# Kernel optimization log

Measured on AMD Instinct MI355X. Metric: run time of the kernel, lower is better.

The kernel has to match this reference:

```python
import jax, jax.numpy as jnp
import numpy as np

N1, N2 = 8192, 8192
E1, E2 = 131072, 131072
F_IN, NH, B = 64, 128, 256
D6 = 6 * NH  # set2set in_channels = 768


def _gcn(x, W, b, src, dst, ew, n):
    xw = x @ W
    loop = jnp.arange(n)
    s = jnp.concatenate([src, loop])
    d = jnp.concatenate([dst, loop])
    w = jnp.concatenate([ew, jnp.ones((n,), ew.dtype)])
    deg = jax.ops.segment_sum(w, d, num_segments=n)
    dinv = jnp.where(deg > 0, jax.lax.rsqrt(deg), 0.0)
    norm = (dinv[s] * w * dinv[d])[:, None]
    return jax.ops.segment_sum(xw[s] * norm, d, num_segments=n) + b


def _leaky(x):
    return jax.nn.leaky_relu(x, 0.2)


def _l2norm(x):
    return x / jnp.maximum(jnp.linalg.norm(x, axis=1, keepdims=True), 1e-12)


def _set2set(x, batch, nseg, Wih, Whh, bih, bhh, steps=2):
    # Set2Set pooling: LSTM(input=2d, hidden=d) + segment softmax attention
    d = x.shape[1]
    h = jnp.zeros((nseg, d), x.dtype)
    c = jnp.zeros((nseg, d), x.dtype)
    q_star = jnp.zeros((nseg, 2 * d), x.dtype)
    for _ in range(steps):
        gates = q_star @ Wih.T + h @ Whh.T + bih + bhh
        gi, gf, gg, go = jnp.split(gates, 4, axis=1)  # torch LSTM gate order i,f,g,o
        c = jax.nn.sigmoid(gf) * c + jax.nn.sigmoid(gi) * jnp.tanh(gg)
        h = jax.nn.sigmoid(go) * jnp.tanh(c)
        e = jnp.sum(x * h[batch], axis=1)
        emax = jax.ops.segment_max(e, batch, num_segments=nseg)
        ee = jnp.exp(e - emax[batch])
        a = ee / jax.ops.segment_sum(ee, batch, num_segments=nseg)[batch]
        r = jax.ops.segment_sum(a[:, None] * x, batch, num_segments=nseg)
        q_star = jnp.concatenate([h, r], axis=1)
    return q_star


def setup_inputs():
    key = jax.random.key(0)
    ks = jax.random.split(key, 20)
    f32 = jnp.float32

    def xav(k, shp):
        fan_in, fan_out = shp[-1], shp[0] if len(shp) == 2 else shp[-1]
        lim = float(np.sqrt(6.0 / (shp[0] + shp[1])))
        return jax.random.uniform(k, shp, f32, -lim, lim)

    inp = {}
    inp["features_1"] = jax.random.normal(ks[0], (N1, F_IN), f32)
    inp["features_2"] = jax.random.normal(ks[1], (N2, F_IN), f32)
    inp["edge_attr_1"] = jax.random.uniform(ks[2], (E1,), f32)
    inp["edge_attr_2"] = jax.random.uniform(ks[3], (E2,), f32)
    inp["W0"] = xav(ks[4], (F_IN, NH)); inp["b0"] = jnp.zeros((NH,), f32)
    inp["W1"] = xav(ks[5], (NH, NH)); inp["b1"] = jnp.zeros((NH,), f32)
    inp["W2"] = xav(ks[6], (NH, NH)); inp["b2"] = jnp.zeros((NH,), f32)
    inp["Wih"] = xav(ks[7], (4 * D6, 2 * D6)); inp["bih"] = jnp.zeros((4 * D6,), f32)
    inp["Whh"] = xav(ks[8], (4 * D6, D6)); inp["bhh"] = jnp.zeros((4 * D6,), f32)
    inp["Wp1"] = xav(ks[9], (256, 4 * D6)); inp["bp1"] = jnp.zeros((256,), f32)
    inp["Wp2"] = xav(ks[10], (128, 256)); inp["bp2"] = jnp.zeros((128,), f32)
    inp["Wp3"] = xav(ks[11], (1, 128)); inp["bp3"] = jnp.zeros((1,), f32)
    inp["edge_index_1"] = jax.random.randint(ks[12], (2, E1), 0, N1)
    inp["edge_index_2"] = jax.random.randint(ks[13], (2, E2), 0, N2)
    inp["batch_1"] = jnp.sort(jax.random.randint(ks[14], (N1,), 0, B))
    inp["batch_2"] = jnp.sort(jax.random.randint(ks[15], (N2,), 0, B))
    return inp


def reference(features_1, features_2, edge_attr_1, edge_attr_2,
              W0, b0, W1, b1, W2, b2, Wih, bih, Whh, bhh,
              Wp1, bp1, Wp2, bp2, Wp3, bp3,
              edge_index_1, edge_index_2, batch_1, batch_2):
    s1, d1 = edge_index_1[0], edge_index_1[1]
    s2, d2 = edge_index_2[0], edge_index_2[1]

    f1a = _leaky(_gcn(features_1, W0, b0, s1, d1, edge_attr_1, N1))
    f2a = _leaky(_gcn(features_2, W0, b0, s2, d2, edge_attr_2, N2))
    f1b = _leaky(_gcn(f1a, W1, b1, s1, d1, edge_attr_1, N1))
    f2b = _leaky(_gcn(f2a, W1, b1, s2, d2, edge_attr_2, N2))
    f1c = _leaky(_gcn(f1b, W2, b2, s1, d1, edge_attr_1, N1))
    f2c = _leaky(_gcn(f2b, W2, b2, s2, d2, edge_attr_2, N2))
    h1 = jnp.concatenate([f1a, f1b, f1c], axis=1)  # [N1, 3*NH]
    h2 = jnp.concatenate([f2a, f2b, f2c], axis=1)  # [N2, 3*NH]

    # interaction: cosine-sim map masked to same-graph pairs (len_map)
    ns = _l2norm(h1)
    nv = _l2norm(h2)
    mask = (batch_1[:, None] == batch_2[None, :]).astype(ns.dtype)  # [N1, N2]
    imap = (ns @ nv.T) * mask
    f1 = jnp.concatenate([ns, imap @ nv], axis=1)      # [N1, 6*NH]
    f2 = jnp.concatenate([nv, imap.T @ ns], axis=1)    # [N2, 6*NH]

    g1 = _set2set(f1, batch_1, B, Wih, Whh, bih, bhh)  # [B, 12*NH]
    g2 = _set2set(f2, batch_2, B, Wih, Whh, bih, bhh)  # [B, 12*NH]
    z = jnp.concatenate([g1, g2], axis=1)              # [B, 24*NH]
    z = jax.nn.relu(z @ Wp1.T + bp1)
    z = jax.nn.relu(z @ Wp2.T + bp2)
    z = z @ Wp3.T + bp3
    return jax.nn.sigmoid(z).reshape(-1)
```

## Files before the change

kernel.cpp:

```cpp
#include <hip/hip_runtime.h>
#include <cmath>

#define N_NODES 8192
#define N_EDGES 131072
#define NB      256
#define NH      128
#define D3      384
#define D6      768
#define SMM     96
#define SLD     104
#define MAXDEG  64

typedef __attribute__((ext_vector_type(8))) short short8v;
typedef __attribute__((ext_vector_type(4))) float f32x4;
typedef unsigned short bf16t;

__device__ __forceinline__ float sigf(float x){ return 1.0f/(1.0f+__expf(-x)); }
__device__ __forceinline__ unsigned short f2bf(float x){
  unsigned u = __float_as_uint(x);
  unsigned r = u + 0x7FFF + ((u>>16)&1);
  return (unsigned short)(r>>16);
}
__device__ __forceinline__ float bfl(unsigned u){ return __uint_as_float(u<<16); }
__device__ __forceinline__ float bfh(unsigned u){ return __uint_as_float(u & 0xFFFF0000u); }
__device__ __forceinline__ float b2f(bf16t u){ return __uint_as_float(((unsigned)u)<<16); }
__device__ __forceinline__ float h0val(const float* bih, const float* bhh, int j){
  float c = sigf(bih[j]+bhh[j]) * tanhf(bih[2*D6+j]+bhh[2*D6+j]);
  return sigf(bih[3*D6+j]+bhh[3*D6+j]) * tanhf(c);
}

__device__ __forceinline__ void xw_body(int vb, int t,
    const bf16t* __restrict__ x1, const bf16t* __restrict__ x2, int xs, int K,
    const bf16t* __restrict__ Wt, bf16t* __restrict__ xw1, bf16t* __restrict__ xw2){
  int side = vb >> 8; int b = vb & 255;
  const bf16t* x = side? x2:x1;
  bf16t* xw = side? xw2:xw1;
  int w = t>>6, lane = t&63;
  int lm = lane&15, quad = lane>>4;
  int r0 = b*32 + (w>>1)*16;
  int c0 = (w&1)*64;
  const bf16t* a = x + (size_t)(r0+lm)*xs + quad*8;
  f32x4 acc[4] = {};
  for (int k=0;k<K;k+=32){
    short8v af = *(const short8v*)(a + k);
    #pragma unroll
    for (int ni=0;ni<4;ni++){
      short8v bf = *(const short8v*)(Wt + (size_t)(c0+ni*16+lm)*K + quad*8 + k);
      acc[ni] = __builtin_amdgcn_mfma_f32_16x16x32_bf16(af, bf, acc[ni], 0,0,0);
    }
  }
  #pragma unroll
  for (int ni=0;ni<4;ni++)
    #pragma unroll
    for (int r=0;r<4;r++){
      int row = r0 + quad*4 + r, col = c0 + ni*16 + lm;
      xw[(size_t)row*NH + col] = f2bf(acc[ni][r]);
    }
}


__global__ __launch_bounds__(256) void k_setup(
    const float* __restrict__ Wih, short* __restrict__ Wih16,
    const float* __restrict__ Wp1, short* __restrict__ Wp116,
    const float* __restrict__ fe1, const float* __restrict__ fe2,
    short* __restrict__ xf1, short* __restrict__ xf2,
    const float* __restrict__ W0, const float* __restrict__ W1, const float* __restrict__ W2,
    bf16t* __restrict__ Wt,
    const float* __restrict__ Whh, const float* __restrict__ bih, const float* __restrict__ bhh,
    float* __restrict__ cvec,
    float* deg1, float* deg2, int* ecur1, int* ecur2, int* cnt1, int* cnt2){
  __shared__ float hs[D6];
  int b = blockIdx.x, tid = threadIdx.x;
  if (b < 2304){
    int t = b*256 + tid;
    int n = t/192, q = t - n*192;
    float4 v = ((const float4*)(Wih + (size_t)n*1536 + 768))[q];
    short4 o = { (short)f2bf(v.x), (short)f2bf(v.y), (short)f2bf(v.z), (short)f2bf(v.w) };
    ((short4*)Wih16)[t] = o;
  } else if (b < 3072){
    int t = (b-2304)*256 + tid;
    float4 v = ((const float4*)Wp1)[t];
    short4 o = { (short)f2bf(v.x), (short)f2bf(v.y), (short)f2bf(v.z), (short)f2bf(v.w) };
    ((short4*)Wp116)[t] = o;
  } else if (b < 4096){
    int t = (b-3072)*256 + tid;
    int side = t >= 131072; int i = t & 131071;
    float4 v = ((const float4*)(side? fe2:fe1))[i];
    short4 o = { (short)f2bf(v.x), (short)f2bf(v.y), (short)f2bf(v.z), (short)f2bf(v.w) };
    ((short4*)(side? xf2:xf1))[i] = o;
  } else if (b < 4099){
    int l = b - 4096;
    const float* W = (l==0)? W0 : ((l==1)? W1 : W2);
    int K = (l==0)? 64 : 128;
    bf16t* dst = Wt + ((l==0)? 0 : ((l==1)? 128*64 : 128*64+128*128));
    for (int idx = tid; idx < 128*K; idx += 256){
      int n = idx / K, k = idx - n*K;
      dst[idx] = f2bf(W[k*NH + n]);
    }
  } else if (b < 4867){
    int j0 = (b - 4099)*4;
    for (int k=tid; k<D6; k+=256) hs[k] = h0val(bih,bhh,k);
    __syncthreads();
    int w = tid>>6, lane = tid&63;
    int j = j0 + w;
    const float4* wi = (const float4*)(Wih + (size_t)j*(2*D6));
    const float4* wh = (const float4*)(Whh + (size_t)j*D6);
    const float4* h4 = (const float4*)hs;
    float acc=0;
    #pragma unroll
    for (int m=0;m<3;m++){
      float4 hv = h4[m*64+lane];
      float4 a = wi[m*64+lane];
      float4 bb = wh[m*64+lane];
      acc += hv.x*(a.x+bb.x) + hv.y*(a.y+bb.y) + hv.z*(a.z+bb.z) + hv.w*(a.w+bb.w);
    }
    #pragma unroll
    for (int m=1;m<64;m<<=1) acc += __shfl_xor(acc,m,64);
    if (lane==0) cvec[j]=acc+bih[j]+bhh[j];
  } else {
    int t = (b-4867)*256 + tid;
    if (t < N_NODES){ deg1[t]=1.f; deg2[t]=1.f; ecur1[t]=0; ecur2[t]=0; }
    if (t < NB){ cnt1[t]=0; cnt2[t]=0; }
  }
}

__global__ __launch_bounds__(256) void k_deg(
    const int* __restrict__ ei1, const float* __restrict__ ea1, float* deg1,
    const int* __restrict__ ei2, const float* __restrict__ ea2, float* deg2,
    const int* __restrict__ b1, const int* __restrict__ b2, int* cnt1, int* cnt2,
    const bf16t* __restrict__ xf1, const bf16t* __restrict__ xf2,
    const bf16t* __restrict__ Wt, bf16t* __restrict__ xwA1, bf16t* __restrict__ xwA2){
  int blk = blockIdx.x;
  if (blk < 1024){
    int idx = blk*256 + threadIdx.x;
    int side = idx >= N_EDGES;
    int e = idx & (N_EDGES-1);
    const int* ei = side? ei2:ei1; const float* ea = side? ea2:ea1;
    float* deg = side? deg2:deg1;
    int d = ei[N_EDGES+e];
    atomicAdd(&deg[d], ea[e]);
    if (idx < N_NODES){ atomicAdd(&cnt1[b1[idx]],1); atomicAdd(&cnt2[b2[idx]],1); }
  } else {
    xw_body(blk-1024, threadIdx.x, xf1, xf2, 64, 64, Wt, xwA1, xwA2);
  }
}

__global__ __launch_bounds__(256) void k_fill(
    const int* __restrict__ ei1, const float* __restrict__ ea1, const float* __restrict__ d1,
    int* cur1, int* es1, float* ec1,
    const int* __restrict__ ei2, const float* __restrict__ ea2, const float* __restrict__ d2,
    int* cur2, int* es2, float* ec2,
    const int* __restrict__ c1, const int* __restrict__ c2, int* st1, int* st2){
  __shared__ int ps[256];
  int blk = blockIdx.x, t = threadIdx.x;
  if (blk < 1024){
    int idx = blk*256 + t;
    int side = idx >= N_EDGES;
    int e = idx & (N_EDGES-1);
    const int* ei = side? ei2:ei1; const float* ea = side? ea2:ea1;
    const float* deg = side? d2:d1;
    int* cur = side? cur2:cur1; int* es = side? es2:es1; float* ec = side? ec2:ec1;
    int s = ei[e], d = ei[N_EDGES+e];
    int pos = atomicAdd(&cur[d], 1);
    if (pos < MAXDEG){
      es[d*MAXDEG + pos] = s;
      ec[d*MAXDEG + pos] = rsqrtf(deg[s])*ea[e]*rsqrtf(deg[d]);
    }
  } else {
    const int* c = (blk==1025)? c2:c1; int* st = (blk==1025)? st2:st1;
    ps[t]=c[t]; __syncthreads();
    for (int d=1; d<256; d<<=1){
      int v = (t>=d)? ps[t-d]:0;
      __syncthreads();
      ps[t]+=v;
      __syncthreads();
    }
    st[t+1]=ps[t];
    if (t==0) st[0]=0;
  }
}


__global__ __launch_bounds__(256) void k_gxw(
    const bf16t* __restrict__ xwi1, const bf16t* __restrict__ xwi2,
    const int* __restrict__ cur1, const int* __restrict__ cur2,
    const int* __restrict__ es1, const int* __restrict__ es2,
    const float* __restrict__ ec1, const float* __restrict__ ec2,
    const float* __restrict__ d1, const float* __restrict__ d2,
    const float* __restrict__ bias, int loff,
    bf16t* __restrict__ h1, bf16t* __restrict__ h2,
    const bf16t* __restrict__ Wl,
    bf16t* __restrict__ xwo1, bf16t* __restrict__ xwo2){
  int blk = blockIdx.x;
  int side = blk >> 9; int b = blk & 511;
  const ushort4* xw = (const ushort4*)(side? xwi2:xwi1);
  const int* cur = side? cur2:cur1;
  const int* es  = side? es2:es1;
  const float* ec= side? ec2:ec1;
  const float* deg = side? d2:d1;
  bf16t* h = side? h2:h1;
  int t = threadIdx.x;
  int c4 = t & 31;
  float4 bv = ((const float4*)bias)[c4];
  #pragma unroll
  for (int grp=0; grp<2; grp++){
    int i = b*16 + grp*8 + (t>>5);
    float sc = 1.0f/deg[i];
    ushort4 v = xw[(size_t)i*32 + c4];
    float4 acc = {b2f(v.x)*sc, b2f(v.y)*sc, b2f(v.z)*sc, b2f(v.w)*sc};
    int r = i*MAXDEG;
    int ce = cur[i]; if (ce > MAXDEG) ce = MAXDEG;
    int r1 = r + ce;
    for (; r+3<r1; r+=4){
      int s0=es[r], s1=es[r+1], s2=es[r+2], s3=es[r+3];
      float w0=ec[r], w1=ec[r+1], w2=ec[r+2], w3=ec[r+3];
      ushort4 u0 = xw[(size_t)s0*32 + c4];
      ushort4 u1 = xw[(size_t)s1*32 + c4];
      ushort4 u2 = xw[(size_t)s2*32 + c4];
      ushort4 u3 = xw[(size_t)s3*32 + c4];
      acc.x += b2f(u0.x)*w0 + b2f(u1.x)*w1 + b2f(u2.x)*w2 + b2f(u3.x)*w3;
      acc.y += b2f(u0.y)*w0 + b2f(u1.y)*w1 + b2f(u2.y)*w2 + b2f(u3.y)*w3;
      acc.z += b2f(u0.z)*w0 + b2f(u1.z)*w1 + b2f(u2.z)*w2 + b2f(u3.z)*w3;
      acc.w += b2f(u0.w)*w0 + b2f(u1.w)*w1 + b2f(u2.w)*w2 + b2f(u3.w)*w3;
    }
    for (; r<r1; r++){
      int s0=es[r]; float w0=ec[r];
      ushort4 u0 = xw[(size_t)s0*32 + c4];
      acc.x+=b2f(u0.x)*w0; acc.y+=b2f(u0.y)*w0; acc.z+=b2f(u0.z)*w0; acc.w+=b2f(u0.w)*w0;
    }
    acc.x+=bv.x; acc.y+=bv.y; acc.z+=bv.z; acc.w+=bv.w;
    acc.x = (acc.x>0.f)?acc.x:0.2f*acc.x;
    acc.y = (acc.y>0.f)?acc.y:0.2f*acc.y;
    acc.z = (acc.z>0.f)?acc.z:0.2f*acc.z;
    acc.w = (acc.w>0.f)?acc.w:0.2f*acc.w;
    ((ushort4*)(h + (size_t)i*D3 + loff))[c4] =
      make_ushort4(f2bf(acc.x), f2bf(acc.y), f2bf(acc.z), f2bf(acc.w));
  }
  __syncthreads();
  int w = t>>6, lane = t&63;
  int lm = lane&15, quad = lane>>4;
  const bf16t* x = (side? h2:h1) + loff;
  int r0 = b*16;
  int c0 = w*32;
  const bf16t* a = x + (size_t)(r0+lm)*D3 + quad*8;
  bf16t* xwo = side? xwo2:xwo1;
  f32x4 acc0={0,0,0,0}, acc1={0,0,0,0};
  for (int k=0;k<128;k+=32){
    short8v af = *(const short8v*)(a + k);
    short8v b0 = *(const short8v*)(Wl + (size_t)(c0+lm)*128 + quad*8 + k);
    short8v b1 = *(const short8v*)(Wl + (size_t)(c0+16+lm)*128 + quad*8 + k);
    acc0 = __builtin_amdgcn_mfma_f32_16x16x32_bf16(af, b0, acc0, 0,0,0);
    acc1 = __builtin_amdgcn_mfma_f32_16x16x32_bf16(af, b1, acc1, 0,0,0);
  }
  #pragma unroll
  for (int r=0;r<4;r++){
    int row = r0 + quad*4 + r;
    xwo[(size_t)row*NH + c0 + lm]      = f2bf(acc0[r]);
    xwo[(size_t)row*NH + c0 + 16 + lm] = f2bf(acc1[r]);
  }
}

__global__ __launch_bounds__(256) void k_gather(const bf16t* __restrict__ xw1, const bf16t* __restrict__ xw2,
                                                const int* __restrict__ cur1, const int* __restrict__ cur2,
                                                const int* __restrict__ es1, const int* __restrict__ es2,
                                                const float* __restrict__ ec1, const float* __restrict__ ec2,
                                                const float* __restrict__ d1, const float* __restrict__ d2,
                                                const float* __restrict__ b,
                                                bf16t* __restrict__ h1, bf16t* __restrict__ h2, int loff,
                                                int l2mode, bf16t* __restrict__ f1, bf16t* __restrict__ f2){
  int blk = blockIdx.x;
  int side = blk >> 10; int bb = blk & 1023;
  const ushort4* xw = (const ushort4*)(side? xw2:xw1);
  const int* cur = side? cur2:cur1;
  const int* es  = side? es2:es1;
  const float* ec= side? ec2:ec1;
  const float* deg = side? d2:d1;
  bf16t* h = side? h2:h1;
  int t = threadIdx.x;
  int i = bb*8 + (t>>5);
  int c4 = t & 31;
  float sc = 1.0f/deg[i];
  ushort4 v = xw[(size_t)i*32 + c4];
  float4 acc = {b2f(v.x)*sc, b2f(v.y)*sc, b2f(v.z)*sc, b2f(v.w)*sc};
  int r = i*MAXDEG;
  int ce = cur[i]; if (ce > MAXDEG) ce = MAXDEG;
  int r1 = r + ce;
  for (; r+3<r1; r+=4){
    int s0=es[r], s1=es[r+1], s2=es[r+2], s3=es[r+3];
    float w0=ec[r], w1=ec[r+1], w2=ec[r+2], w3=ec[r+3];
    ushort4 u0 = xw[(size_t)s0*32 + c4];
    ushort4 u1 = xw[(size_t)s1*32 + c4];
    ushort4 u2 = xw[(size_t)s2*32 + c4];
    ushort4 u3 = xw[(size_t)s3*32 + c4];
    acc.x += b2f(u0.x)*w0 + b2f(u1.x)*w1 + b2f(u2.x)*w2 + b2f(u3.x)*w3;
    acc.y += b2f(u0.y)*w0 + b2f(u1.y)*w1 + b2f(u2.y)*w2 + b2f(u3.y)*w3;
    acc.z += b2f(u0.z)*w0 + b2f(u1.z)*w1 + b2f(u2.z)*w2 + b2f(u3.z)*w3;
    acc.w += b2f(u0.w)*w0 + b2f(u1.w)*w1 + b2f(u2.w)*w2 + b2f(u3.w)*w3;
  }
  for (; r<r1; r++){
    int s0=es[r]; float w0=ec[r];
    ushort4 u0 = xw[(size_t)s0*32 + c4];
    acc.x+=b2f(u0.x)*w0; acc.y+=b2f(u0.y)*w0; acc.z+=b2f(u0.z)*w0; acc.w+=b2f(u0.w)*w0;
  }
  float4 bv = ((const float4*)b)[c4];
  acc.x+=bv.x; acc.y+=bv.y; acc.z+=bv.z; acc.w+=bv.w;
  acc.x = (acc.x>0.f)?acc.x:0.2f*acc.x;
  acc.y = (acc.y>0.f)?acc.y:0.2f*acc.y;
  acc.z = (acc.z>0.f)?acc.z:0.2f*acc.z;
  acc.w = (acc.w>0.f)?acc.w:0.2f*acc.w;
  if (!l2mode){
    ((ushort4*)(h + (size_t)i*D3 + loff))[c4] =
      make_ushort4(f2bf(acc.x), f2bf(acc.y), f2bf(acc.z), f2bf(acc.w));
  } else {
    ushort4 u0 = ((const ushort4*)(h + (size_t)i*D3))[c4];
    ushort4 u1 = ((const ushort4*)(h + (size_t)i*D3 + 128))[c4];
    float4 v0 = {b2f(u0.x), b2f(u0.y), b2f(u0.z), b2f(u0.w)};
    float4 v1 = {b2f(u1.x), b2f(u1.y), b2f(u1.z), b2f(u1.w)};
    float ss = v0.x*v0.x+v0.y*v0.y+v0.z*v0.z+v0.w*v0.w
             + v1.x*v1.x+v1.y*v1.y+v1.z*v1.z+v1.w*v1.w
             + acc.x*acc.x+acc.y*acc.y+acc.z*acc.z+acc.w*acc.w;
    #pragma unroll
    for (int m=1;m<32;m<<=1) ss += __shfl_xor(ss, m, 64);
    float scale = 1.0f/fmaxf(sqrtf(ss), 1e-12f);
    bf16t* f = side? f2:f1;
    ((ushort4*)(f + (size_t)i*D6))[c4]       = make_ushort4(f2bf(v0.x*scale),f2bf(v0.y*scale),f2bf(v0.z*scale),f2bf(v0.w*scale));
    ((ushort4*)(f + (size_t)i*D6 + 128))[c4] = make_ushort4(f2bf(v1.x*scale),f2bf(v1.y*scale),f2bf(v1.z*scale),f2bf(v1.w*scale));
    ((ushort4*)(f + (size_t)i*D6 + 256))[c4] = make_ushort4(f2bf(acc.x*scale),f2bf(acc.y*scale),f2bf(acc.z*scale),f2bf(acc.w*scale));
  }
}

__global__ __launch_bounds__(256) void k_inter(bf16t* __restrict__ f1, bf16t* __restrict__ f2,
                                               const int* __restrict__ st1, const int* __restrict__ st2,
                                               const float* __restrict__ bih, const float* __restrict__ bhh,
                                               bf16t* __restrict__ Ab){
  __shared__ __align__(16) bf16t Sld[SMM*SLD];
  __shared__ bf16t tbuf[32*392];
  int bx = blockIdx.x;
  int side = bx >> 8, g = bx & (NB-1);
  int i0 = st1[g]; int n1 = st1[g+1]-i0; if (n1>SMM) n1=SMM;
  int j0 = st2[g]; int n2 = st2[g+1]-j0; if (n2>SMM) n2=SMM;
  int cnt = side? n2 : n1;
  int J   = side? n1 : n2;
  int r0base = side? j0 : i0;
  int c0base = side? i0 : j0;
  const bf16t* rowp = (side? f2 : f1);
  const bf16t* colp = (side? f1 : f2);
  const bf16t* src = colp + (size_t)c0base*D6;
  bf16t* dst = (side? f2 : f1) + (size_t)r0base*D6 + D3;
  int t = threadIdx.x, w = t>>6, lane = t&63;
  int lm = lane & 15, quad = lane >> 4;
  {
    uint4* z1 = (uint4*)Sld;
    uint4 zz = make_uint4(0,0,0,0);
    for (int i=t; i<1248; i+=256) z1[i]=zz;
  }
  __syncthreads();
  int nti = (cnt+15)>>4, ntj = (J+15)>>4;
  for (int tile = w; tile < nti*ntj; tile += 4){
    int ti = tile/ntj, tj = tile - ti*ntj;
    int ar = r0base + ti*16 + lm; if (ar > N_NODES-1) ar = N_NODES-1;
    int br = c0base + tj*16 + lm; if (br > N_NODES-1) br = N_NODES-1;
    const bf16t* a = rowp + (size_t)ar*D6 + quad*8;
    const bf16t* b = colp + (size_t)br*D6 + quad*8;
    f32x4 acc = {0,0,0,0};
    #pragma unroll
    for (int k=0; k<384; k+=32){
      short8v af = *(const short8v*)(a + k);
      short8v bf = *(const short8v*)(b + k);
      acc = __builtin_amdgcn_mfma_f32_16x16x32_bf16(af, bf, acc, 0, 0, 0);
    }
    int col = tj*16 + lm;
    #pragma unroll
    for (int r=0;r<4;r++){
      int row = ti*16 + quad*4 + r;
      if (row < cnt && col < J)
        Sld[row*SLD + col] = f2bf(acc[r]);
    }
  }
  __syncthreads();
  for (int r0=0; r0<cnt; r0+=32){
    int mt1 = (cnt - r0 > 16) ? 2 : 1;
    f32x4 acc[2][6] = {};
    for (int kb = 0; kb < J; kb += 32){
      __syncthreads();
      for (int idx = t; idx < 32*48; idx += 256){
        int j = idx/48, cg2 = idx - j*48;
        uint4 v = (kb+j < J)? ((const uint4*)(src + (size_t)(kb+j)*D6))[cg2] : make_uint4(0,0,0,0);
        *(uint4*)(tbuf + j*392 + cg2*8) = v;
      }
      const bf16t* ap = Sld + (r0 + lm)*SLD + kb + quad*8;
      short8v af0 = *(const short8v*)ap;
      short8v af1 = (mt1 > 1)? *(const short8v*)(ap + 16*SLD) : af0;
      __syncthreads();
      #pragma unroll
      for (int ni = 0; ni < 6; ni++){
        int nt = w*6 + ni;
        short8v bf;
        #pragma unroll
        for (int ji = 0; ji < 8; ji++)
          bf[ji] = (short)tbuf[(quad*8 + ji)*392 + nt*16 + lm];
        acc[0][ni] = __builtin_amdgcn_mfma_f32_16x16x32_bf16(af0, bf, acc[0][ni], 0, 0, 0);
        if (mt1 > 1)
          acc[1][ni] = __builtin_amdgcn_mfma_f32_16x16x32_bf16(af1, bf, acc[1][ni], 0, 0, 0);
      }
    }
    for (int mt = 0; mt < mt1; mt++)
      for (int ni = 0; ni < 6; ni++){
        int nt = w*6 + ni;
        #pragma unroll
        for (int r = 0; r < 4; r++){
          int row = r0 + mt*16 + quad*4 + r;
          if (row < cnt) dst[(size_t)row*D6 + nt*16 + lm] = f2bf(acc[mt][ni][r]);
        }
      }
  }
  __syncthreads();
  {
    float4* hs = (float4*)Sld;
    float* e_s = ((float*)Sld) + 768;
    float* part = ((float*)Sld) + 864;
    const bf16t* x = rowp + (size_t)r0base*D6;
    if (t<192){
      int j = t*4;
      hs[t] = make_float4(h0val(bih,bhh,j), h0val(bih,bhh,j+1), h0val(bih,bhh,j+2), h0val(bih,bhh,j+3));
    }
    __syncthreads();
    for (int n=w; n<cnt; n+=4){
      const uint2* xr = (const uint2*)(x + (size_t)n*D6);
      float p = 0;
      #pragma unroll
      for (int m=0;m<3;m++){
        uint2 rv = xr[m*64+lane];
        float4 hvv = hs[m*64+lane];
        p += bfl(rv.x)*hvv.x + bfh(rv.x)*hvv.y + bfl(rv.y)*hvv.z + bfh(rv.y)*hvv.w;
      }
      #pragma unroll
      for (int m=1;m<64;m<<=1) p += __shfl_xor(p,m,64);
      if (lane==0) e_s[n]=p;
    }
    __syncthreads();
    if (w==0){
      float mx=-INFINITY;
      for (int n=lane;n<cnt;n+=64) mx=fmaxf(mx,e_s[n]);
      #pragma unroll
      for (int m=1;m<64;m<<=1) mx=fmaxf(mx,__shfl_xor(mx,m,64));
      float s=0;
      for (int n=lane;n<cnt;n+=64) s+=__expf(e_s[n]-mx);
      #pragma unroll
      for (int m=1;m<64;m<<=1) s+=__shfl_xor(s,m,64);
      float inv=1.0f/s;
      for (int n=lane;n<cnt;n+=64) e_s[n]=__expf(e_s[n]-mx)*inv;
    }
    __syncthreads();
    float av[3][4] = {};
    for (int n=w; n<cnt; n+=4){
      float a = e_s[n];
      const uint2* xr = (const uint2*)(x + (size_t)n*D6);
      #pragma unroll
      for (int m=0;m<3;m++){
        uint2 rv = xr[m*64+lane];
        av[m][0]+=a*bfl(rv.x); av[m][1]+=a*bfh(rv.x); av[m][2]+=a*bfl(rv.y); av[m][3]+=a*bfh(rv.y);
      }
    }
    #pragma unroll
    for (int m=0;m<3;m++)
      *(float4*)&part[w*D6 + (m*64+lane)*4] = make_float4(av[m][0],av[m][1],av[m][2],av[m][3]);
    __syncthreads();
    if (t<192){
      float4 p0 = *(const float4*)&part[0*D6 + t*4];
      float4 p1 = *(const float4*)&part[1*D6 + t*4];
      float4 p2 = *(const float4*)&part[2*D6 + t*4];
      float4 p3 = *(const float4*)&part[3*D6 + t*4];
      float4 s = make_float4(p0.x+p1.x+p2.x+p3.x, p0.y+p1.y+p2.y+p3.y,
                             p0.z+p1.z+p2.z+p3.z, p0.w+p1.w+p2.w+p3.w);
      ushort4 o = make_ushort4(f2bf(s.x), f2bf(s.y), f2bf(s.z), f2bf(s.w));
      ((ushort4*)(Ab + (size_t)(side*NB+g)*D6))[t]=o;
    }
  }
}


__global__ __launch_bounds__(256) void k_att(const bf16t* __restrict__ f1, const bf16t* __restrict__ f2,
                                             const float* __restrict__ hbase, int perseg,
                                             const float* __restrict__ bih, const float* __restrict__ bhh,
                                             const int* __restrict__ st1, const int* __restrict__ st2,
                                             bf16t* __restrict__ dst16, long sidestep, long dstride){
  __shared__ float4 hs[192];
  __shared__ float e_s[SMM];
  __shared__ float part[4][D6];
  int side = blockIdx.x >> 8, g = blockIdx.x & (NB-1);
  const int* st = side? st2:st1;
  int n0 = st[g]; int cnt = st[g+1]-n0; if (cnt>SMM) cnt=SMM;
  const bf16t* x = (side? f2:f1) + (size_t)n0*D6;
  int t = threadIdx.x, w = t>>6, lane = t&63;
  if (t<192){
    if (perseg){
      hs[t] = ((const float4*)(hbase + (size_t)(side*NB+g)*D6))[t];
    } else {
      int j = t*4;
      hs[t] = make_float4(h0val(bih,bhh,j), h0val(bih,bhh,j+1), h0val(bih,bhh,j+2), h0val(bih,bhh,j+3));
    }
  }
  __syncthreads();
  for (int n=w; n<cnt; n+=4){
    const uint2* xr = (const uint2*)(x + (size_t)n*D6);
    float p = 0;
    #pragma unroll
    for (int m=0;m<3;m++){
      uint2 rv = xr[m*64+lane];
      float4 hvv = hs[m*64+lane];
      p += bfl(rv.x)*hvv.x + bfh(rv.x)*hvv.y + bfl(rv.y)*hvv.z + bfh(rv.y)*hvv.w;
    }
    #pragma unroll
    for (int m=1;m<64;m<<=1) p += __shfl_xor(p,m,64);
    if (lane==0) e_s[n]=p;
  }
  __syncthreads();
  if (w==0){
    float mx=-INFINITY;
    for (int n=lane;n<cnt;n+=64) mx=fmaxf(mx,e_s[n]);
    #pragma unroll
    for (int m=1;m<64;m<<=1) mx=fmaxf(mx,__shfl_xor(mx,m,64));
    float s=0;
    for (int n=lane;n<cnt;n+=64) s+=__expf(e_s[n]-mx);
    #pragma unroll
    for (int m=1;m<64;m<<=1) s+=__shfl_xor(s,m,64);
    float inv=1.0f/s;
    for (int n=lane;n<cnt;n+=64) e_s[n]=__expf(e_s[n]-mx)*inv;
  }
  __syncthreads();
  float av[3][4] = {};
  for (int n=w; n<cnt; n+=4){
    float a = e_s[n];
    const uint2* xr = (const uint2*)(x + (size_t)n*D6);
    #pragma unroll
    for (int m=0;m<3;m++){
      uint2 rv = xr[m*64+lane];
      av[m][0]+=a*bfl(rv.x); av[m][1]+=a*bfh(rv.x); av[m][2]+=a*bfl(rv.y); av[m][3]+=a*bfh(rv.y);
    }
  }
  #pragma unroll
  for (int m=0;m<3;m++)
    *(float4*)&part[w][(m*64+lane)*4] = make_float4(av[m][0],av[m][1],av[m][2],av[m][3]);
  __syncthreads();
  if (t<192){
    float4 p0 = *(const float4*)&part[0][t*4];
    float4 p1 = *(const float4*)&part[1][t*4];
    float4 p2 = *(const float4*)&part[2][t*4];
    float4 p3 = *(const float4*)&part[3][t*4];
    float4 s = make_float4(p0.x+p1.x+p2.x+p3.x, p0.y+p1.y+p2.y+p3.y,
                           p0.z+p1.z+p2.z+p3.z, p0.w+p1.w+p2.w+p3.w);
    ushort4 o = make_ushort4(f2bf(s.x), f2bf(s.y), f2bf(s.z), f2bf(s.w));
    ushort4* dp = (ushort4*)(dst16 + side*sidestep + (size_t)g*dstride);
    dp[t]=o;
  }
}

__global__ __launch_bounds__(256) void k_gates(const short* __restrict__ A16,
                                               const short* __restrict__ B16,
                                               const float* __restrict__ cvec,
                                               const float* __restrict__ bih, const float* __restrict__ bhh,
                                               float* __restrict__ h1s, bf16t* __restrict__ z16){
  __shared__ float gbuf[4][16][66];
  int w = threadIdx.x >> 6, lane = threadIdx.x & 63;
  int lm = lane & 15, quad = lane >> 4;
  int bm = blockIdx.x * 16;
  int jb = blockIdx.y * 64;
  const short* a = A16 + (size_t)(bm + lm)*768 + quad*8;
  const short* b = B16 + (size_t)(w*768 + jb + lm)*768 + quad*8;
  f32x4 acc0={0,0,0,0}, acc1={0,0,0,0}, acc2={0,0,0,0}, acc3={0,0,0,0};
  for (int k=0; k<768; k+=32){
    short8v af = *(const short8v*)(a + k);
    short8v b0 = *(const short8v*)(b + k);
    short8v b1 = *(const short8v*)(b + 16*768 + k);
    short8v b2 = *(const short8v*)(b + 32*768 + k);
    short8v b3 = *(const short8v*)(b + 48*768 + k);
    acc0 = __builtin_amdgcn_mfma_f32_16x16x32_bf16(af, b0, acc0, 0, 0, 0);
    acc1 = __builtin_amdgcn_mfma_f32_16x16x32_bf16(af, b1, acc1, 0, 0, 0);
    acc2 = __builtin_amdgcn_mfma_f32_16x16x32_bf16(af, b2, acc2, 0, 0, 0);
    acc3 = __builtin_amdgcn_mfma_f32_16x16x32_bf16(af, b3, acc3, 0, 0, 0);
  }
  #pragma unroll
  for (int r=0;r<4;r++){
    gbuf[w][quad*4+r][lm]      = acc0[r];
    gbuf[w][quad*4+r][16+lm]   = acc1[r];
    gbuf[w][quad*4+r][32+lm]   = acc2[r];
    gbuf[w][quad*4+r][48+lm]   = acc3[r];
  }
  __syncthreads();
  int t = threadIdx.x;
  #pragma unroll
  for (int u=0; u<4; u++){
    int p = t + u*256;
    int mm = p>>6, jj = p&63;
    int j = jb + jj, m = bm + mm;
    float g4[4];
    #pragma unroll
    for (int q=0;q<4;q++) g4[q] = gbuf[q][mm][jj] + cvec[q*D6 + j];
    float c0j = sigf(bih[j]+bhh[j]) * tanhf(bih[2*D6+j]+bhh[2*D6+j]);
    float c = sigf(g4[1])*c0j + sigf(g4[0])*tanhf(g4[2]);
    float h = sigf(g4[3])*tanhf(c);
    h1s[(size_t)m*D6 + j] = h;
    int side = m>>8, g = m&255;
    z16[(size_t)g*3072 + side*1536 + j] = f2bf(h);
  }
}

__global__ __launch_bounds__(256) void k_gemm_mfma_p1(const short* __restrict__ A16,
                                                      const short* __restrict__ B16,
                                                      float* __restrict__ pout){
  int w = threadIdx.x >> 6, lane = threadIdx.x & 63;
  int lm = lane & 15, quad = lane >> 4;
  int bm = blockIdx.x * 16;
  int bn = w * 64;
  int kbase = blockIdx.y * 192;
  const short* a = A16 + (size_t)(bm + lm)*3072 + quad*8 + kbase;
  const short* b = B16 + (size_t)(bn + lm)*3072 + quad*8 + kbase;
  f32x4 acc0={0,0,0,0}, acc1={0,0,0,0}, acc2={0,0,0,0}, acc3={0,0,0,0};
  for (int k=0; k<192; k+=32){
    short8v af = *(const short8v*)(a + k);
    short8v b0 = *(const short8v*)(b + k);
    short8v b1 = *(const short8v*)(b + 16*3072 + k);
    short8v b2 = *(const short8v*)(b + 32*3072 + k);
    short8v b3 = *(const short8v*)(b + 48*3072 + k);
    acc0 = __builtin_amdgcn_mfma_f32_16x16x32_bf16(af, b0, acc0, 0, 0, 0);
    acc1 = __builtin_amdgcn_mfma_f32_16x16x32_bf16(af, b1, acc1, 0, 0, 0);
    acc2 = __builtin_amdgcn_mfma_f32_16x16x32_bf16(af, b2, acc2, 0, 0, 0);
    acc3 = __builtin_amdgcn_mfma_f32_16x16x32_bf16(af, b3, acc3, 0, 0, 0);
  }
  float* po = pout + (size_t)blockIdx.y*256*256;
  #pragma unroll
  for (int r=0;r<4;r++){
    size_t base = (size_t)(bm + quad*4 + r)*256 + bn + lm;
    po[base]      = acc0[r];
    po[base + 16] = acc1[r];
    po[base + 32] = acc2[r];
    po[base + 48] = acc3[r];
  }
}

__global__ __launch_bounds__(128) void k_p23(const float* __restrict__ pbuf, const float* __restrict__ bp1,
                                             const float* __restrict__ Wp2, const float* __restrict__ bp2,
                                             const float* __restrict__ Wp3, const float* __restrict__ bp3,
                                             float* __restrict__ out){
  __shared__ float zr[256];
  __shared__ float ws[2];
  int m = blockIdx.x, t = threadIdx.x;
  float2 zacc = ((const float2*)(bp1))[t];
  #pragma unroll
  for (int p=0;p<16;p++){
    float2 v = ((const float2*)(pbuf + (size_t)p*256*256 + (size_t)m*256))[t];
    zacc.x += v.x; zacc.y += v.y;
  }
  zr[2*t]   = fmaxf(zacc.x, 0.f);
  zr[2*t+1] = fmaxf(zacc.y, 0.f);
  __syncthreads();
  const float4* wrow = (const float4*)(Wp2 + (size_t)t*256);
  const float4* z4 = (const float4*)zr;
  float acc = bp2[t];
  #pragma unroll 8
  for (int k=0;k<64;k++){
    float4 wv = wrow[k], zv = z4[k];
    acc += wv.x*zv.x + wv.y*zv.y + wv.z*zv.z + wv.w*zv.w;
  }
  float p = fmaxf(acc,0.f)*Wp3[t];
  #pragma unroll
  for (int o=32;o;o>>=1) p += __shfl_down(p,o,64);
  if ((t&63)==0) ws[t>>6]=p;
  __syncthreads();
  if (t==0){ float v=ws[0]+ws[1]+bp3[0]; out[m]=1.0f/(1.0f+__expf(-v)); }
}


extern "C" void kernel_launch(void* const* d_in, const int* in_sizes, int n_in,
                              void* d_out, int out_size, void* d_ws, size_t ws_size,
                              hipStream_t stream){
  const float* feat1=(const float*)d_in[0];
  const float* feat2=(const float*)d_in[1];
  const float* ea1  =(const float*)d_in[2];
  const float* ea2  =(const float*)d_in[3];
  const float* W0=(const float*)d_in[4];  const float* b0=(const float*)d_in[5];
  const float* W1=(const float*)d_in[6];  const float* b1=(const float*)d_in[7];
  const float* W2=(const float*)d_in[8];  const float* b2=(const float*)d_in[9];
  const float* Wih=(const float*)d_in[10]; const float* bih=(const float*)d_in[11];
  const float* Whh=(const float*)d_in[12]; const float* bhh=(const float*)d_in[13];
  const float* Wp1=(const float*)d_in[14]; const float* bp1=(const float*)d_in[15];
  const float* Wp2=(const float*)d_in[16]; const float* bp2=(const float*)d_in[17];
  const float* Wp3=(const float*)d_in[18]; const float* bp3=(const float*)d_in[19];
  const int* ei1=(const int*)d_in[20]; const int* ei2=(const int*)d_in[21];
  const int* batch1=(const int*)d_in[22]; const int* batch2=(const int*)d_in[23];
  float* out = (float*)d_out;

  float* base = (float*)d_ws;
  size_t off = 0;
  auto alloc = [&](size_t n)->float* { float* r = base + off; off += (n + 255) & ~(size_t)255; return r; };
  float* deg1 = alloc(N_NODES);          float* deg2 = alloc(N_NODES);
  bf16t* xwA1 = (bf16t*)alloc((size_t)N_NODES*NH/2);
  bf16t* xwA2 = (bf16t*)alloc((size_t)N_NODES*NH/2);
  bf16t* xwB1 = (bf16t*)alloc((size_t)N_NODES*NH/2);
  bf16t* xwB2 = (bf16t*)alloc((size_t)N_NODES*NH/2);
  bf16t* hb1  = (bf16t*)alloc((size_t)N_NODES*D3/2);
  bf16t* hb2  = (bf16t*)alloc((size_t)N_NODES*D3/2);
  bf16t* xf1  = (bf16t*)alloc((size_t)N_NODES*64/2);
  bf16t* xf2  = (bf16t*)alloc((size_t)N_NODES*64/2);
  bf16t* Wtb  = (bf16t*)alloc((size_t)(128*64 + 2*128*128)/2);
  bf16t* f1   = (bf16t*)alloc((size_t)N_NODES*D6/2);
  bf16t* f2   = (bf16t*)alloc((size_t)N_NODES*D6/2);
  float* ecoef1 = alloc((size_t)N_NODES*MAXDEG);  float* ecoef2 = alloc((size_t)N_NODES*MAXDEG);
  float* cvec = alloc(4*D6);
  float* h1s  = alloc((size_t)512*D6);
  bf16t* zbuf16 = (bf16t*)alloc((size_t)256*3072/2);
  float* pbuf = alloc((size_t)16*256*256);
  short* Abuf16 = (short*)alloc((size_t)512*D6/2);
  short* Wih16  = (short*)alloc((size_t)3072*D6/2);
  short* Wp116  = (short*)alloc((size_t)256*3072/2);
  int* cnt1 = (int*)alloc(NB);   int* cnt2 = (int*)alloc(NB);
  int* st1  = (int*)alloc(NB+1); int* st2  = (int*)alloc(NB+1);
  int* ecur1= (int*)alloc(N_NODES); int* ecur2 = (int*)alloc(N_NODES);
  int* esrc1= (int*)alloc((size_t)N_NODES*MAXDEG); int* esrc2 = (int*)alloc((size_t)N_NODES*MAXDEG);
  (void)ws_size; (void)in_sizes; (void)n_in; (void)out_size;

  k_setup  <<<4899,256,0,stream>>>(Wih,Wih16, Wp1,Wp116, feat1,feat2,(short*)xf1,(short*)xf2,
                                   W0,W1,W2,Wtb, Whh,bih,bhh, cvec,
                                   deg1,deg2,ecur1,ecur2,cnt1,cnt2);
  k_deg    <<<1536,256,0,stream>>>(ei1,ea1,deg1, ei2,ea2,deg2, batch1,batch2,cnt1,cnt2,
                                   xf1,xf2,Wtb,xwA1,xwA2);
  k_fill   <<<1026,256,0,stream>>>(ei1,ea1,deg1,ecur1,esrc1,ecoef1,
                                   ei2,ea2,deg2,ecur2,esrc2,ecoef2,
                                   cnt1,cnt2,st1,st2);

  const bf16t* Wt1 = Wtb + 128*64;
  const bf16t* Wt2 = Wtb + 128*64 + 128*128;
  k_gxw<<<1024,256,0,stream>>>(xwA1,xwA2, ecur1,ecur2, esrc1,esrc2, ecoef1,ecoef2,
                               deg1,deg2, b0, 0, hb1,hb2, Wt1, xwB1,xwB2);
  k_gxw<<<1024,256,0,stream>>>(xwB1,xwB2, ecur1,ecur2, esrc1,esrc2, ecoef1,ecoef2,
                               deg1,deg2, b1, NH, hb1,hb2, Wt2, xwA1,xwA2);
  k_gather <<<2048,256,0,stream>>>(xwA1,xwA2,ecur1,ecur2,esrc1,esrc2,ecoef1,ecoef2,
                                   deg1,deg2,b2,hb1,hb2,2*NH,1,f1,f2);

  k_inter <<<512,256,0,stream>>>(f1,f2,st1,st2,bih,bhh,(bf16t*)Abuf16);

  k_gates<<<dim3(32,12),256,0,stream>>>(Abuf16, Wih16, cvec, bih, bhh, h1s, zbuf16);

  k_att<<<512,256,0,stream>>>(f1,f2,h1s,1,bih,bhh,st1,st2,
                              zbuf16+768,(long)1536,(long)3072);

  k_gemm_mfma_p1<<<dim3(16,16),256,0,stream>>>((const short*)zbuf16, Wp116, pbuf);
  k_p23 <<<256,128,0,stream>>>(pbuf, bp1, Wp2, bp2, Wp3, bp3, out);
}
```

Measured before the change: 327.3 us.

## Build CSR first, compute degree from buckets, fold normalization into first GCN layer

The edge bucketing (atomic position plus source and raw weight) now runs in the first pass alongside the first XW GEMM, which removes the separate float-atomic degree pass. A small kernel then computes each node's degree by summing its bucketed edge weights and also does the batch prefix scan. The symmetric normalization coefficients are computed lazily in the first gather layer, which writes them back for later layers. This saves one full edge pass and its atomics, but adds per-edge deg lookups and rsqrt in layer one, and the degree kernel uses one thread per node with serial strided reads.

After: 322.2 us. About the same (-1.5%).

```diff
diff --git a/kernel.cpp b/kernel.cpp
--- a/kernel.cpp
+++ b/kernel.cpp
@@ -68,7 +68,7 @@
     bf16t* __restrict__ Wt,
     const float* __restrict__ Whh, const float* __restrict__ bih, const float* __restrict__ bhh,
     float* __restrict__ cvec,
-    float* deg1, float* deg2, int* ecur1, int* ecur2, int* cnt1, int* cnt2){
+    int* ecur1, int* ecur2, int* cnt1, int* cnt2){
   __shared__ float hs[D6];
   int b = blockIdx.x, tid = threadIdx.x;
   if (b < 2304){
@@ -119,14 +119,15 @@
     if (lane==0) cvec[j]=acc+bih[j]+bhh[j];
   } else {
     int t = (b-4867)*256 + tid;
-    if (t < N_NODES){ deg1[t]=1.f; deg2[t]=1.f; ecur1[t]=0; ecur2[t]=0; }
+    if (t < N_NODES){ ecur1[t]=0; ecur2[t]=0; }
     if (t < NB){ cnt1[t]=0; cnt2[t]=0; }
   }
 }
 
-__global__ __launch_bounds__(256) void k_deg(
-    const int* __restrict__ ei1, const float* __restrict__ ea1, float* deg1,
-    const int* __restrict__ ei2, const float* __restrict__ ea2, float* deg2,
+__global__ __launch_bounds__(256) void k_fill2(
+    const int* __restrict__ ei1, const float* __restrict__ ea1,
+    const int* __restrict__ ei2, const float* __restrict__ ea2,
+    int* cur1, int* es1, float* ec1, int* cur2, int* es2, float* ec2,
     const int* __restrict__ b1, const int* __restrict__ b2, int* cnt1, int* cnt2,
     const bf16t* __restrict__ xf1, const bf16t* __restrict__ xf2,
     const bf16t* __restrict__ Wt, bf16t* __restrict__ xwA1, bf16t* __restrict__ xwA2){
@@ -136,38 +137,39 @@
     int side = idx >= N_EDGES;
     int e = idx & (N_EDGES-1);
     const int* ei = side? ei2:ei1; const float* ea = side? ea2:ea1;
-    float* deg = side? deg2:deg1;
-    int d = ei[N_EDGES+e];
-    atomicAdd(&deg[d], ea[e]);
-    if (idx < N_NODES){ atomicAdd(&cnt1[b1[idx]],1); atomicAdd(&cnt2[b2[idx]],1); }
-  } else {
-    xw_body(blk-1024, threadIdx.x, xf1, xf2, 64, 64, Wt, xwA1, xwA2);
-  }
-}
-
-__global__ __launch_bounds__(256) void k_fill(
-    const int* __restrict__ ei1, const float* __restrict__ ea1, const float* __restrict__ d1,
-    int* cur1, int* es1, float* ec1,
-    const int* __restrict__ ei2, const float* __restrict__ ea2, const float* __restrict__ d2,
-    int* cur2, int* es2, float* ec2,
-    const int* __restrict__ c1, const int* __restrict__ c2, int* st1, int* st2){
-  __shared__ int ps[256];
-  int blk = blockIdx.x, t = threadIdx.x;
-  if (blk < 1024){
-    int idx = blk*256 + t;
-    int side = idx >= N_EDGES;
-    int e = idx & (N_EDGES-1);
-    const int* ei = side? ei2:ei1; const float* ea = side? ea2:ea1;
-    const float* deg = side? d2:d1;
     int* cur = side? cur2:cur1; int* es = side? es2:es1; float* ec = side? ec2:ec1;
     int s = ei[e], d = ei[N_EDGES+e];
     int pos = atomicAdd(&cur[d], 1);
     if (pos < MAXDEG){
       es[d*MAXDEG + pos] = s;
-      ec[d*MAXDEG + pos] = rsqrtf(deg[s])*ea[e]*rsqrtf(deg[d]);
-    }
+      ec[d*MAXDEG + pos] = ea[e];
+    }
+    if (idx < N_NODES){ atomicAdd(&cnt1[b1[idx]],1); atomicAdd(&cnt2[b2[idx]],1); }
   } else {
-    const int* c = (blk==1025)? c2:c1; int* st = (blk==1025)? st2:st1;
+    xw_body(blk-1024, threadIdx.x, xf1, xf2, 64, 64, Wt, xwA1, xwA2);
+  }
+}
+
+__global__ __launch_bounds__(256) void k_deg2(
+    const int* __restrict__ cur1, const float* __restrict__ ec1, float* deg1,
+    const int* __restrict__ cur2, const float* __restrict__ ec2, float* deg2,
+    const int* __restrict__ c1, const int* __restrict__ c2, int* st1, int* st2){
+  __shared__ int ps[256];
+  int blk = blockIdx.x, t = threadIdx.x;
+  if (blk < 64){
+    int idx = blk*256 + t;
+    int side = idx >= N_NODES;
+    int i = idx & (N_NODES-1);
+    const int* cur = side? cur2:cur1;
+    const float* ec = side? ec2:ec1;
+    float* deg = side? deg2:deg1;
+    int ce = cur[i]; if (ce > MAXDEG) ce = MAXDEG;
+    float s = 1.0f;
+    const float* p = ec + (size_t)i*MAXDEG;
+    for (int k=0;k<ce;k++) s += p[k];
+    deg[i] = s;
+  } else {
+    const int* c = (blk==65)? c2:c1; int* st = (blk==65)? st2:st1;
     ps[t]=c[t]; __syncthreads();
     for (int d=1; d<256; d<<=1){
       int v = (t>=d)? ps[t-d]:0;
@@ -185,9 +187,9 @@
     const bf16t* __restrict__ xwi1, const bf16t* __restrict__ xwi2,
     const int* __restrict__ cur1, const int* __restrict__ cur2,
     const int* __restrict__ es1, const int* __restrict__ es2,
-    const float* __restrict__ ec1, const float* __restrict__ ec2,
+    float* __restrict__ ec1, float* __restrict__ ec2,
     const float* __restrict__ d1, const float* __restrict__ d2,
-    const float* __restrict__ bias, int loff,
+    const float* __restrict__ bias, int loff, int coefmode,
     bf16t* __restrict__ h1, bf16t* __restrict__ h2,
     const bf16t* __restrict__ Wl,
     bf16t* __restrict__ xwo1, bf16t* __restrict__ xwo2){
@@ -196,7 +198,7 @@
   const ushort4* xw = (const ushort4*)(side? xwi2:xwi1);
   const int* cur = side? cur2:cur1;
   const int* es  = side? es2:es1;
-  const float* ec= side? ec2:ec1;
+  float* ec = side? ec2:ec1;
   const float* deg = side? d2:d1;
   bf16t* h = side? h2:h1;
   int t = threadIdx.x;
@@ -205,7 +207,9 @@
   #pragma unroll
   for (int grp=0; grp<2; grp++){
     int i = b*16 + grp*8 + (t>>5);
-    float sc = 1.0f/deg[i];
+    float dgi = deg[i];
+    float sc = 1.0f/dgi;
+    float rsq_d = rsqrtf(dgi);
     ushort4 v = xw[(size_t)i*32 + c4];
     float4 acc = {b2f(v.x)*sc, b2f(v.y)*sc, b2f(v.z)*sc, b2f(v.w)*sc};
     int r = i*MAXDEG;
@@ -214,6 +218,13 @@
     for (; r+3<r1; r+=4){
       int s0=es[r], s1=es[r+1], s2=es[r+2], s3=es[r+3];
       float w0=ec[r], w1=ec[r+1], w2=ec[r+2], w3=ec[r+3];
+      if (coefmode){
+        w0 *= rsqrtf(deg[s0])*rsq_d;
+        w1 *= rsqrtf(deg[s1])*rsq_d;
+        w2 *= rsqrtf(deg[s2])*rsq_d;
+        w3 *= rsqrtf(deg[s3])*rsq_d;
+        if (c4==0){ ec[r]=w0; ec[r+1]=w1; ec[r+2]=w2; ec[r+3]=w3; }
+      }
       ushort4 u0 = xw[(size_t)s0*32 + c4];
       ushort4 u1 = xw[(size_t)s1*32 + c4];
       ushort4 u2 = xw[(size_t)s2*32 + c4];
@@ -225,6 +236,10 @@
     }
     for (; r<r1; r++){
       int s0=es[r]; float w0=ec[r];
+      if (coefmode){
+        w0 *= rsqrtf(deg[s0])*rsq_d;
+        if (c4==0) ec[r]=w0;
+      }
       ushort4 u0 = xw[(size_t)s0*32 + c4];
       acc.x+=b2f(u0.x)*w0; acc.y+=b2f(u0.y)*w0; acc.z+=b2f(u0.z)*w0; acc.w+=b2f(u0.w)*w0;
     }
@@ -722,19 +737,20 @@
 
   k_setup  <<<4899,256,0,stream>>>(Wih,Wih16, Wp1,Wp116, feat1,feat2,(short*)xf1,(short*)xf2,
                                    W0,W1,W2,Wtb, Whh,bih,bhh, cvec,
-                                   deg1,deg2,ecur1,ecur2,cnt1,cnt2);
-  k_deg    <<<1536,256,0,stream>>>(ei1,ea1,deg1, ei2,ea2,deg2, batch1,batch2,cnt1,cnt2,
+                                   ecur1,ecur2,cnt1,cnt2);
+  k_fill2  <<<1536,256,0,stream>>>(ei1,ea1, ei2,ea2,
+                                   ecur1,esrc1,ecoef1, ecur2,esrc2,ecoef2,
+                                   batch1,batch2,cnt1,cnt2,
                                    xf1,xf2,Wtb,xwA1,xwA2);
-  k_fill   <<<1026,256,0,stream>>>(ei1,ea1,deg1,ecur1,esrc1,ecoef1,
-                                   ei2,ea2,deg2,ecur2,esrc2,ecoef2,
-                                   cnt1,cnt2,st1,st2);
+  k_deg2   <<<66,256,0,stream>>>(ecur1,ecoef1,deg1, ecur2,ecoef2,deg2,
+                                 cnt1,cnt2,st1,st2);
 
   const bf16t* Wt1 = Wtb + 128*64;
   const bf16t* Wt2 = Wtb + 128*64 + 128*128;
   k_gxw<<<1024,256,0,stream>>>(xwA1,xwA2, ecur1,ecur2, esrc1,esrc2, ecoef1,ecoef2,
-                               deg1,deg2, b0, 0, hb1,hb2, Wt1, xwB1,xwB2);
+                               deg1,deg2, b0, 0, 1, hb1,hb2, Wt1, xwB1,xwB2);
   k_gxw<<<1024,256,0,stream>>>(xwB1,xwB2, ecur1,ecur2, esrc1,esrc2, ecoef1,ecoef2,
-                               deg1,deg2, b1, NH, hb1,hb2, Wt2, xwA1,xwA2);
+                               deg1,deg2, b1, NH, 0, hb1,hb2, Wt2, xwA1,xwA2);
   k_gather <<<2048,256,0,stream>>>(xwA1,xwA2,ecur1,ecur2,esrc1,esrc2,ecoef1,ecoef2,
                                    deg1,deg2,b2,hb1,hb2,2*NH,1,f1,f2);
 
```
